# Kernel tuning notes

Measured on AMD Instinct MI355X. Metric: run time of the kernel, lower is better.

The kernel has to match this reference:

```python
import jax, jax.numpy as jnp
import numpy as np

B, C_IN, C_OUT, H, W = 16, 256, 256, 64, 64
RANK, ORDER = 16, 2
EPS = 1e-5


def setup_inputs() -> dict:
    key = jax.random.key(0)
    k1, k2, k3 = jax.random.split(key, 3)
    x = jax.random.normal(k1, (B, C_IN, H, W), dtype=jnp.float32)
    # torch init: w_core ~ N(0, 1/(C_in*rank)), w_out ~ N(0, 1/rank)
    w_core = jax.random.normal(k2, (RANK, C_IN, RANK), dtype=jnp.float32) * (1.0 / (C_IN * RANK))
    w_out = jax.random.normal(k3, (RANK, C_OUT, RANK), dtype=jnp.float32) * (1.0 / RANK)
    return {"x": x, "w_core": w_core, "w_out": w_out}


def reference(x, w_core, w_out):
    # Per-pixel tensor-ring 1x1 conv.
    # Original chain for order=2 (share_core):
    #   T = einsum('achw,rck->arhwk', x, w_core)
    #   out = einsum('aebcf,afbcg,gdh->aedbch', T, T, w_out)
    #   y   = einsum('arohwr->aohw', out)   # ring trace over e==h
    # Equivalent: M[a,h,w] is rank x rank; P = M^order; y_d = tr(P @ W_d)
    M = jnp.einsum('achw,rck->ahwrk', x, w_core)  # [B,H,W,r,r]
    P = M
    for _ in range(ORDER - 1):
        P = jnp.einsum('ahwef,ahwfg->ahweg', P, M)
    y = jnp.einsum('ahweg,gde->adhw', P, w_out)  # [B,C_out,H,W]
    # InstanceNorm2d (affine=False, biased variance) + Softsign
    mean = jnp.mean(y, axis=(2, 3), keepdims=True)
    var = jnp.var(y, axis=(2, 3), keepdims=True)
    yn = (y - mean) * jax.lax.rsqrt(var + EPS)
    return yn / (1.0 + jnp.abs(yn))
```

## Files before the change

kernel.cpp:

```cpp
#include <hip/hip_runtime.h>

#define HW 4096
#define NC 256
#define ND 256
#define NB 16

typedef _Float16 half2_t __attribute__((ext_vector_type(2)));
typedef _Float16 half4_t __attribute__((ext_vector_type(4)));
typedef _Float16 half8_t __attribute__((ext_vector_type(8)));
typedef __fp16   fp16x2  __attribute__((ext_vector_type(2)));
typedef float floatx2 __attribute__((ext_vector_type(2)));
typedef float floatx4 __attribute__((ext_vector_type(4)));

#define MSCALE 64.0f
#define INV_MSCALE2 (1.0f / 4096.0f)
#define EPS_SCALED (1e-5f * 4096.0f * 4096.0f)

__global__ __launch_bounds__(256) void prep_weights(
        const float* __restrict__ w_core, const float* __restrict__ w_out,
        _Float16* __restrict__ W1p, _Float16* __restrict__ W2p,
        float* __restrict__ ssum) {
    int tid = blockIdx.x * 256 + threadIdx.x;
    if (tid < 8192) ssum[tid] = 0.f;
    int l   = tid & 63;
    int rt  = (tid >> 6) & 15;
    int ks  = (tid >> 10) & 7;
    int sel = tid >> 13;
    int row = l & 15, kg = l >> 4;
    half8_t v;
    if (sel == 0) {
        int r = rt, k = row;
#pragma unroll
        for (int j = 0; j < 8; ++j) {
            int c = ks * 32 + kg * 8 + j;
            v[j] = (_Float16)(w_core[r * 4096 + c * 16 + k] * MSCALE);
        }
        *(half8_t*)&W1p[(size_t)((ks * 16 + rt) * 64 + l) * 8] = v;
    } else {
        int d = rt * 16 + row;
#pragma unroll
        for (int j = 0; j < 8; ++j) {
            int eg = ks * 32 + kg * 8 + j, e = eg >> 4, g = eg & 15;
            v[j] = (_Float16)w_out[g * 4096 + d * 16 + e];
        }
        *(half8_t*)&W2p[(size_t)((ks * 16 + rt) * 64 + l) * 8] = v;
    }
}

template<bool F16Y>
__global__ __launch_bounds__(256, 3) void compute_y(
        const float* __restrict__ x, const _Float16* __restrict__ W1p,
        const _Float16* __restrict__ W2p, float* __restrict__ y,
        _Float16* __restrict__ y16, float* __restrict__ ssum,
        float* __restrict__ ssq) {
    __shared__ __align__(16) _Float16 S[16384];

    const int t = threadIdx.x;
    const int l = t & 63, w = t >> 6;
    const int a = blockIdx.x >> 6;
    const int pixbase = (blockIdx.x & 63) * 64;
    const int row16 = l & 15, kg = l >> 4;
    const float* xa = x + (size_t)a * NC * HW + pixbase;

    const half8_t* W1v = (const half8_t*)W1p;
    half8_t af[4], afn[4];
#pragma unroll
    for (int rq = 0; rq < 4; ++rq) af[rq] = W1v[(w * 4 + rq) * 64 + l];

    {
        const int px = t & 63;
        const int o0 = t >> 6;
#pragma unroll
        for (int h = 0; h < 2; ++h) {
            float xr[32];
#pragma unroll
            for (int q = 0; q < 4; ++q) {
                const int oct = (h * 4 + q) * 4 + o0;
#pragma unroll
                for (int j = 0; j < 8; ++j)
                    xr[q * 8 + j] = xa[(size_t)(oct * 8 + j) * HW + px];
            }
#pragma unroll
            for (int q = 0; q < 4; ++q) {
                const int oct = (h * 4 + q) * 4 + o0;
                half8_t hv;
#pragma unroll
                for (int j = 0; j < 8; ++j) hv[j] = (_Float16)xr[q * 8 + j];
                *(half8_t*)&S[px * 256 + ((oct ^ (px & 15)) << 3)] = hv;
            }
        }
    }
    __syncthreads();

    floatx4 acc[4][4];
#pragma unroll
    for (int i = 0; i < 4; ++i)
#pragma unroll
        for (int j = 0; j < 4; ++j) acc[i][j] = (floatx4){0.f, 0.f, 0.f, 0.f};
    for (int ks = 0; ks < 8; ++ks) {
        if (ks < 7) {
#pragma unroll
            for (int rq = 0; rq < 4; ++rq)
                afn[rq] = W1v[((ks + 1) * 16 + w * 4 + rq) * 64 + l];
        }
#pragma unroll
        for (int pt = 0; pt < 4; ++pt) {
            const int px = pt * 16 + row16;
            half8_t bf = *(const half8_t*)
                &S[px * 256 + (((ks * 4 + kg) ^ row16) << 3)];
#pragma unroll
            for (int rq = 0; rq < 4; ++rq)
                acc[rq][pt] = __builtin_amdgcn_mfma_f32_16x16x32_f16(
                                  af[rq], bf, acc[rq][pt], 0, 0, 0);
        }
#pragma unroll
        for (int rq = 0; rq < 4; ++rq) af[rq] = afn[rq];
    }

    const half8_t* W2v = (const half8_t*)W2p;
    half8_t caf[4], cafn[4];
#pragma unroll
    for (int dq = 0; dq < 4; ++dq) caf[dq] = W2v[(w * 4 + dq) * 64 + l];

    __syncthreads();

#pragma unroll
    for (int rq = 0; rq < 4; ++rq) {
        const int u = (w * 4 + rq) * 4 + kg;
#pragma unroll
        for (int pt = 0; pt < 4; ++pt) {
            const int px = pt * 16 + row16;
            half4_t hv;
#pragma unroll
            for (int r2 = 0; r2 < 4; ++r2) hv[r2] = (_Float16)acc[rq][pt][r2];
            *(half4_t*)&S[px * 256 + ((u ^ row16) << 2)] = hv;
        }
    }
    __syncthreads();

    {
        const int p = t >> 2, qe = t & 3, ps = p & 15;
        const _Float16* Mp = &S[p * 256];
        floatx2 Pacc[4][8];
#pragma unroll
        for (int i = 0; i < 4; ++i)
#pragma unroll
            for (int g2 = 0; g2 < 8; ++g2) Pacc[i][g2] = (floatx2){0.f, 0.f};
#pragma unroll
        for (int f4 = 0; f4 < 4; ++f4) {
            float Afb[4][4];
#pragma unroll
            for (int i = 0; i < 4; ++i) {
                const int e = i * 4 + qe;
                half4_t v = *(const half4_t*)
                    &Mp[(((e * 4 + f4) ^ ps) << 2)];
#pragma unroll
                for (int j = 0; j < 4; ++j) Afb[i][j] = (float)v[j];
            }
#pragma unroll
            for (int fl = 0; fl < 4; ++fl) {
                const int f = f4 * 4 + fl;
                floatx2 Bg[8];
#pragma unroll
                for (int g4 = 0; g4 < 4; ++g4) {
                    half4_t v = *(const half4_t*)
                        &Mp[(((f * 4 + g4) ^ ps) << 2)];
                    Bg[g4 * 2]     = (floatx2){(float)v[0], (float)v[1]};
                    Bg[g4 * 2 + 1] = (floatx2){(float)v[2], (float)v[3]};
                }
#pragma unroll
                for (int i = 0; i < 4; ++i) {
                    floatx2 a2 = {Afb[i][fl], Afb[i][fl]};
#pragma unroll
                    for (int g2 = 0; g2 < 8; ++g2)
                        Pacc[i][g2] = __builtin_elementwise_fma(a2, Bg[g2],
                                                                Pacc[i][g2]);
                }
            }
        }
#pragma unroll
        for (int i = 0; i < 4; ++i) {
            const int e = i * 4 + qe;
#pragma unroll
            for (int h2 = 0; h2 < 2; ++h2) {
                half8_t hv;
#pragma unroll
                for (int g2 = 0; g2 < 4; ++g2) {
                    fp16x2 pk = __builtin_amdgcn_cvt_pkrtz(
                        Pacc[i][h2 * 4 + g2][0], Pacc[i][h2 * 4 + g2][1]);
                    hv[g2 * 2]     = (_Float16)pk[0];
                    hv[g2 * 2 + 1] = (_Float16)pk[1];
                }
                *(half8_t*)&S[p * 256 + (((e * 2 + h2) ^ ps) << 3)] = hv;
            }
        }
    }
    __syncthreads();

    floatx4 cacc[4][4];
#pragma unroll
    for (int i = 0; i < 4; ++i)
#pragma unroll
        for (int j = 0; j < 4; ++j) cacc[i][j] = (floatx4){0.f, 0.f, 0.f, 0.f};
    for (int ks = 0; ks < 8; ++ks) {
        if (ks < 7) {
#pragma unroll
            for (int dq = 0; dq < 4; ++dq)
                cafn[dq] = W2v[((ks + 1) * 16 + w * 4 + dq) * 64 + l];
        }
#pragma unroll
        for (int pt = 0; pt < 4; ++pt) {
            const int px = pt * 16 + row16;
            half8_t bf = *(const half8_t*)
                &S[px * 256 + (((ks * 4 + kg) ^ row16) << 3)];
#pragma unroll
            for (int dq = 0; dq < 4; ++dq)
                cacc[dq][pt] = __builtin_amdgcn_mfma_f32_16x16x32_f16(
                                   caf[dq], bf, cacc[dq][pt], 0, 0, 0);
        }
#pragma unroll
        for (int dq = 0; dq < 4; ++dq) caf[dq] = cafn[dq];
    }

    float*     ya   = y   + (size_t)a * ND * HW + pixbase;
    _Float16*  ya16 = F16Y ? (y16 + (size_t)a * ND * HW + pixbase) : nullptr;
#pragma unroll
    for (int dq = 0; dq < 4; ++dq) {
        const int dbase = (w * 4 + dq) * 16 + kg * 4;
#pragma unroll
        for (int r2 = 0; r2 < 4; ++r2) {
            const int d = dbase + r2;
            float s = 0.f, q2 = 0.f;
#pragma unroll
            for (int pt = 0; pt < 4; ++pt) {
                float v;
                if (F16Y) {
                    _Float16 hv = (_Float16)cacc[dq][pt][r2];
                    ya16[(size_t)d * HW + pt * 16 + row16] = hv;
                    v = (float)hv;
                } else {
                    v = cacc[dq][pt][r2] * INV_MSCALE2;
                    ya[(size_t)d * HW + pt * 16 + row16] = v;
                }
                s += v; q2 += v * v;
            }
#pragma unroll
            for (int off = 1; off < 16; off <<= 1) {
                s  += __shfl_xor(s, off);
                q2 += __shfl_xor(q2, off);
            }
            if (row16 == 0) {
                atomicAdd(&ssum[a * 256 + d], s);
                atomicAdd(&ssq [a * 256 + d], q2);
            }
        }
    }
}

__global__ __launch_bounds__(256) void finalize_f16(
        const _Float16* __restrict__ y16, const float* __restrict__ ssum,
        const float* __restrict__ ssq, float* __restrict__ out) {
    const int ad = blockIdx.x;
    const float m  = ssum[ad] * (1.f / HW);
    const float sv = ssq[ad] * (1.f / HW) - m * m;
    const float s  = rsqrtf(sv + EPS_SCALED);
    const size_t base = (size_t)ad * HW + threadIdx.x * 16;
    half8_t h0 = *(const half8_t*)&y16[base];
    half8_t h1 = *(const half8_t*)&y16[base + 8];
    float o[16];
#pragma unroll
    for (int j = 0; j < 8; ++j) {
        float z0 = ((float)h0[j] - m) * s;
        float z1 = ((float)h1[j] - m) * s;
        o[j]     = z0 / (1.f + fabsf(z0));
        o[8 + j] = z1 / (1.f + fabsf(z1));
    }
#pragma unroll
    for (int q = 0; q < 4; ++q)
        *(float4*)&out[base + q * 4] =
            make_float4(o[q * 4], o[q * 4 + 1], o[q * 4 + 2], o[q * 4 + 3]);
}

__global__ __launch_bounds__(256) void finalize_f32(
        float* __restrict__ y, const float* __restrict__ ssum,
        const float* __restrict__ ssq) {
    const int i4 = blockIdx.x * 256 + threadIdx.x;
    const int ad = i4 >> 10;
    const float m  = ssum[ad] * (1.f / HW);
    const float sv = ssq[ad] * (1.f / HW) - m * m;
    const float s  = rsqrtf(sv + 1e-5f);
    float4 v = ((const float4*)y)[i4];
    float vv[4] = {v.x, v.y, v.z, v.w};
#pragma unroll
    for (int lq = 0; lq < 4; ++lq) {
        float z = (vv[lq] - m) * s;
        vv[lq] = z / (1.f + fabsf(z));
    }
    ((float4*)y)[i4] = make_float4(vv[0], vv[1], vv[2], vv[3]);
}

extern "C" void kernel_launch(void* const* d_in, const int* in_sizes, int n_in,
                              void* d_out, int out_size, void* d_ws, size_t ws_size,
                              hipStream_t stream) {
    const float* x      = (const float*)d_in[0];
    const float* w_core = (const float*)d_in[1];
    const float* w_out  = (const float*)d_in[2];
    float* y = (float*)d_out;

    char* wsb = (char*)d_ws;
    _Float16* W1p = (_Float16*)wsb;
    _Float16* W2p = (_Float16*)(wsb + 131072);
    float* ssum   = (float*)(wsb + 262144);
    float* ssq    = (float*)(wsb + 278528);
    _Float16* y16 = (_Float16*)(wsb + 294912);

    const size_t need_f16 = 294912 + (size_t)NB * ND * HW * sizeof(_Float16);
    const bool use_f16 = ws_size >= need_f16;

    prep_weights<<<64, 256, 0, stream>>>(w_core, w_out, W1p, W2p, ssum);
    if (use_f16) {
        compute_y<true><<<1024, 256, 0, stream>>>(x, W1p, W2p, y, y16, ssum, ssq);
        finalize_f16<<<4096, 256, 0, stream>>>(y16, ssum, ssq, y);
    } else {
        compute_y<false><<<1024, 256, 0, stream>>>(x, W1p, W2p, y, nullptr, ssum, ssq);
        finalize_f32<<<16384, 256, 0, stream>>>(y, ssum, ssq);
    }
}
```

Before: 90.77 us.

## Restructure compute_y as single-wave blocks of 16 pixels without barriers

The compute kernel changes from 256-thread blocks handling 64 pixels to 64-thread single-wave blocks handling 16 pixels, launched on a 4x larger grid. Each wave loads its x tile straight into registers as MFMA B fragments, so the shared-memory staging of x and all __syncthreads barriers go away. LDS use drops to 8 KB per block. The trade-off is that every block now reloads the full W1/W2 weight fragments for only 16 pixels, which raises weight traffic and issues four times as many atomics per channel. The x global loads also become 16-pixel (64-byte) segments per channel instead of 256-byte ones.

```diff
diff --git a/kernel.cpp b/kernel.cpp
--- a/kernel.cpp
+++ b/kernel.cpp
@@ -5,7 +5,6 @@
 #define ND 256
 #define NB 16
 
-typedef _Float16 half2_t __attribute__((ext_vector_type(2)));
 typedef _Float16 half4_t __attribute__((ext_vector_type(4)));
 typedef _Float16 half8_t __attribute__((ext_vector_type(8)));
 typedef __fp16   fp16x2  __attribute__((ext_vector_type(2)));
@@ -48,98 +47,70 @@
 }
 
 template<bool F16Y>
-__global__ __launch_bounds__(256, 3) void compute_y(
+__global__ __launch_bounds__(64) void compute_y(
         const float* __restrict__ x, const _Float16* __restrict__ W1p,
         const _Float16* __restrict__ W2p, float* __restrict__ y,
         _Float16* __restrict__ y16, float* __restrict__ ssum,
         float* __restrict__ ssq) {
-    __shared__ __align__(16) _Float16 S[16384];
+    __shared__ __align__(16) _Float16 S[4096];
 
     const int t = threadIdx.x;
-    const int l = t & 63, w = t >> 6;
-    const int a = blockIdx.x >> 6;
-    const int pixbase = (blockIdx.x & 63) * 64;
-    const int row16 = l & 15, kg = l >> 4;
-    const float* xa = x + (size_t)a * NC * HW + pixbase;
+    const int a = blockIdx.x >> 8;
+    const int pixbase = (blockIdx.x & 255) * 16;
+    const int row16 = t & 15, kg = t >> 4;
+    const float* xa = x + (size_t)a * NC * HW + pixbase + row16;
+
+    half8_t bx[8];
+#pragma unroll
+    for (int ks = 0; ks < 8; ++ks) {
+        float xr[8];
+#pragma unroll
+        for (int j = 0; j < 8; ++j)
+            xr[j] = xa[(size_t)(ks * 32 + kg * 8 + j) * HW];
+#pragma unroll
+        for (int j = 0; j < 8; ++j) bx[ks][j] = (_Float16)xr[j];
+    }
 
     const half8_t* W1v = (const half8_t*)W1p;
-    half8_t af[4], afn[4];
-#pragma unroll
-    for (int rq = 0; rq < 4; ++rq) af[rq] = W1v[(w * 4 + rq) * 64 + l];
-
     {
-        const int px = t & 63;
-        const int o0 = t >> 6;
-#pragma unroll
-        for (int h = 0; h < 2; ++h) {
-            float xr[32];
-#pragma unroll
-            for (int q = 0; q < 4; ++q) {
-                const int oct = (h * 4 + q) * 4 + o0;
-#pragma unroll
-                for (int j = 0; j < 8; ++j)
-                    xr[q * 8 + j] = xa[(size_t)(oct * 8 + j) * HW + px];
-            }
-#pragma unroll
-            for (int q = 0; q < 4; ++q) {
-                const int oct = (h * 4 + q) * 4 + o0;
-                half8_t hv;
-#pragma unroll
-                for (int j = 0; j < 8; ++j) hv[j] = (_Float16)xr[q * 8 + j];
-                *(half8_t*)&S[px * 256 + ((oct ^ (px & 15)) << 3)] = hv;
-            }
-        }
-    }
-    __syncthreads();
-
-    floatx4 acc[4][4];
-#pragma unroll
-    for (int i = 0; i < 4; ++i)
-#pragma unroll
-        for (int j = 0; j < 4; ++j) acc[i][j] = (floatx4){0.f, 0.f, 0.f, 0.f};
-    for (int ks = 0; ks < 8; ++ks) {
-        if (ks < 7) {
-#pragma unroll
-            for (int rq = 0; rq < 4; ++rq)
-                afn[rq] = W1v[((ks + 1) * 16 + w * 4 + rq) * 64 + l];
-        }
-#pragma unroll
-        for (int pt = 0; pt < 4; ++pt) {
-            const int px = pt * 16 + row16;
-            half8_t bf = *(const half8_t*)
-                &S[px * 256 + (((ks * 4 + kg) ^ row16) << 3)];
-#pragma unroll
-            for (int rq = 0; rq < 4; ++rq)
-                acc[rq][pt] = __builtin_amdgcn_mfma_f32_16x16x32_f16(
-                                  af[rq], bf, acc[rq][pt], 0, 0, 0);
-        }
-#pragma unroll
-        for (int rq = 0; rq < 4; ++rq) af[rq] = afn[rq];
-    }
-
-    const half8_t* W2v = (const half8_t*)W2p;
-    half8_t caf[4], cafn[4];
-#pragma unroll
-    for (int dq = 0; dq < 4; ++dq) caf[dq] = W2v[(w * 4 + dq) * 64 + l];
-
-    __syncthreads();
-
-#pragma unroll
-    for (int rq = 0; rq < 4; ++rq) {
-        const int u = (w * 4 + rq) * 4 + kg;
-#pragma unroll
-        for (int pt = 0; pt < 4; ++pt) {
-            const int px = pt * 16 + row16;
-            half4_t hv;
-#pragma unroll
-            for (int r2 = 0; r2 < 4; ++r2) hv[r2] = (_Float16)acc[rq][pt][r2];
-            *(half4_t*)&S[px * 256 + ((u ^ row16) << 2)] = hv;
-        }
-    }
-    __syncthreads();
+        half8_t af[4], afn[4];
+#pragma unroll
+        for (int rq = 0; rq < 4; ++rq) af[rq] = W1v[rq * 64 + t];
+#pragma unroll
+        for (int rtg = 0; rtg < 4; ++rtg) {
+            floatx4 acc[4];
+#pragma unroll
+            for (int rq = 0; rq < 4; ++rq) acc[rq] = (floatx4){0.f,0.f,0.f,0.f};
+#pragma unroll
+            for (int ks = 0; ks < 8; ++ks) {
+                const bool last = (rtg == 3) && (ks == 7);
+                const int nrtg = (ks == 7) ? rtg + 1 : rtg;
+                const int nks  = (ks == 7) ? 0 : ks + 1;
+                if (!last) {
+#pragma unroll
+                    for (int rq = 0; rq < 4; ++rq)
+                        afn[rq] = W1v[(nks * 16 + nrtg * 4 + rq) * 64 + t];
+                }
+#pragma unroll
+                for (int rq = 0; rq < 4; ++rq)
+                    acc[rq] = __builtin_amdgcn_mfma_f32_16x16x32_f16(
+                                  af[rq], bx[ks], acc[rq], 0, 0, 0);
+#pragma unroll
+                for (int rq = 0; rq < 4; ++rq) af[rq] = afn[rq];
+            }
+#pragma unroll
+            for (int rq = 0; rq < 4; ++rq) {
+                const int u = (rtg * 4 + rq) * 4 + kg;
+                half4_t hv;
+#pragma unroll
+                for (int r2 = 0; r2 < 4; ++r2) hv[r2] = (_Float16)acc[rq][r2];
+                *(half4_t*)&S[row16 * 256 + ((u ^ row16) << 2)] = hv;
+            }
+        }
+    }
 
     {
-        const int p = t >> 2, qe = t & 3, ps = p & 15;
+        const int p = t >> 2, qe = t & 3, ps = p;
         const _Float16* Mp = &S[p * 256];
         floatx2 Pacc[4][8];
 #pragma unroll
@@ -152,8 +123,7 @@
 #pragma unroll
             for (int i = 0; i < 4; ++i) {
                 const int e = i * 4 + qe;
-                half4_t v = *(const half4_t*)
-                    &Mp[(((e * 4 + f4) ^ ps) << 2)];
+                half4_t v = *(const half4_t*)&Mp[(((e * 4 + f4) ^ ps) << 2)];
 #pragma unroll
                 for (int j = 0; j < 4; ++j) Afb[i][j] = (float)v[j];
             }
@@ -195,63 +165,64 @@
             }
         }
     }
-    __syncthreads();
-
-    floatx4 cacc[4][4];
-#pragma unroll
-    for (int i = 0; i < 4; ++i)
-#pragma unroll
-        for (int j = 0; j < 4; ++j) cacc[i][j] = (floatx4){0.f, 0.f, 0.f, 0.f};
-    for (int ks = 0; ks < 8; ++ks) {
-        if (ks < 7) {
-#pragma unroll
-            for (int dq = 0; dq < 4; ++dq)
-                cafn[dq] = W2v[((ks + 1) * 16 + w * 4 + dq) * 64 + l];
-        }
-#pragma unroll
-        for (int pt = 0; pt < 4; ++pt) {
-            const int px = pt * 16 + row16;
-            half8_t bf = *(const half8_t*)
-                &S[px * 256 + (((ks * 4 + kg) ^ row16) << 3)];
-#pragma unroll
-            for (int dq = 0; dq < 4; ++dq)
-                cacc[dq][pt] = __builtin_amdgcn_mfma_f32_16x16x32_f16(
-                                   caf[dq], bf, cacc[dq][pt], 0, 0, 0);
-        }
-#pragma unroll
-        for (int dq = 0; dq < 4; ++dq) caf[dq] = cafn[dq];
-    }
-
-    float*     ya   = y   + (size_t)a * ND * HW + pixbase;
-    _Float16*  ya16 = F16Y ? (y16 + (size_t)a * ND * HW + pixbase) : nullptr;
-#pragma unroll
-    for (int dq = 0; dq < 4; ++dq) {
-        const int dbase = (w * 4 + dq) * 16 + kg * 4;
-#pragma unroll
-        for (int r2 = 0; r2 < 4; ++r2) {
-            const int d = dbase + r2;
-            float s = 0.f, q2 = 0.f;
-#pragma unroll
-            for (int pt = 0; pt < 4; ++pt) {
-                float v;
-                if (F16Y) {
-                    _Float16 hv = (_Float16)cacc[dq][pt][r2];
-                    ya16[(size_t)d * HW + pt * 16 + row16] = hv;
-                    v = (float)hv;
-                } else {
-                    v = cacc[dq][pt][r2] * INV_MSCALE2;
-                    ya[(size_t)d * HW + pt * 16 + row16] = v;
-                }
-                s += v; q2 += v * v;
-            }
-#pragma unroll
-            for (int off = 1; off < 16; off <<= 1) {
-                s  += __shfl_xor(s, off);
-                q2 += __shfl_xor(q2, off);
-            }
-            if (row16 == 0) {
-                atomicAdd(&ssum[a * 256 + d], s);
-                atomicAdd(&ssq [a * 256 + d], q2);
+
+    const half8_t* W2v = (const half8_t*)W2p;
+    float*    ya   = y   + (size_t)a * ND * HW + pixbase;
+    _Float16* ya16 = F16Y ? (y16 + (size_t)a * ND * HW + pixbase) : nullptr;
+    {
+        half8_t caf[4], cafn[4];
+#pragma unroll
+        for (int dq = 0; dq < 4; ++dq) caf[dq] = W2v[dq * 64 + t];
+#pragma unroll
+        for (int dtg = 0; dtg < 4; ++dtg) {
+            floatx4 cacc[4];
+#pragma unroll
+            for (int dq = 0; dq < 4; ++dq) cacc[dq] = (floatx4){0.f,0.f,0.f,0.f};
+#pragma unroll
+            for (int ks = 0; ks < 8; ++ks) {
+                const bool last = (dtg == 3) && (ks == 7);
+                const int ndtg = (ks == 7) ? dtg + 1 : dtg;
+                const int nks  = (ks == 7) ? 0 : ks + 1;
+                if (!last) {
+#pragma unroll
+                    for (int dq = 0; dq < 4; ++dq)
+                        cafn[dq] = W2v[(nks * 16 + ndtg * 4 + dq) * 64 + t];
+                }
+                half8_t bf = *(const half8_t*)
+                    &S[row16 * 256 + (((ks * 4 + kg) ^ row16) << 3)];
+#pragma unroll
+                for (int dq = 0; dq < 4; ++dq)
+                    cacc[dq] = __builtin_amdgcn_mfma_f32_16x16x32_f16(
+                                   caf[dq], bf, cacc[dq], 0, 0, 0);
+#pragma unroll
+                for (int dq = 0; dq < 4; ++dq) caf[dq] = cafn[dq];
+            }
+#pragma unroll
+            for (int dq = 0; dq < 4; ++dq) {
+                const int dbase = (dtg * 4 + dq) * 16 + kg * 4;
+#pragma unroll
+                for (int r2 = 0; r2 < 4; ++r2) {
+                    const int d = dbase + r2;
+                    float v;
+                    if (F16Y) {
+                        _Float16 hv = (_Float16)cacc[dq][r2];
+                        ya16[(size_t)d * HW + row16] = hv;
+                        v = (float)hv;
+                    } else {
+                        v = cacc[dq][r2] * INV_MSCALE2;
+                        ya[(size_t)d * HW + row16] = v;
+                    }
+                    float s = v, q2 = v * v;
+#pragma unroll
+                    for (int off = 1; off < 16; off <<= 1) {
+                        s  += __shfl_xor(s, off);
+                        q2 += __shfl_xor(q2, off);
+                    }
+                    if (row16 == 0) {
+                        atomicAdd(&ssum[a * 256 + d], s);
+                        atomicAdd(&ssq [a * 256 + d], q2);
+                    }
+                }
             }
         }
     }
@@ -319,10 +290,10 @@
 
     prep_weights<<<64, 256, 0, stream>>>(w_core, w_out, W1p, W2p, ssum);
     if (use_f16) {
-        compute_y<true><<<1024, 256, 0, stream>>>(x, W1p, W2p, y, y16, ssum, ssq);
+        compute_y<true><<<4096, 64, 0, stream>>>(x, W1p, W2p, y, y16, ssum, ssq);
         finalize_f16<<<4096, 256, 0, stream>>>(y16, ssum, ssq, y);
     } else {
-        compute_y<false><<<1024, 256, 0, stream>>>(x, W1p, W2p, y, nullptr, ssum, ssq);
+        compute_y<false><<<4096, 64, 0, stream>>>(x, W1p, W2p, y, nullptr, ssum, ssq);
         finalize_f32<<<16384, 256, 0, stream>>>(y, ssum, ssq);
     }
 }
```

Result: slower. 169.4 us (+86.6%).
